# Optimization experiments

Measured on AMD Instinct MI355X. Metric: run time of the kernel, lower is better.

Reference implementation:

```python
import jax, jax.numpy as jnp
import numpy as np

NUM_UNITS = 64
IN_FEATURES = 256
OUT_FEATURES = 256


def _uw(x, w):
    # per-unit linear: x [B,U,I], w [U,I,O] -> [B,U,O]
    return jnp.einsum('bui,uio->buo', x, w)


def setup_inputs() -> dict:
    key = jax.random.key(0)
    ks = jax.random.split(key, 8)
    bound = float(np.sqrt(1.0 / OUT_FEATURES))
    U, I, O = NUM_UNITS, IN_FEATURES, OUT_FEATURES
    B = 256
    uni = lambda k, s: jax.random.uniform(k, s, jnp.float32, -bound, bound)
    return {
        'x': jax.random.normal(ks[0], (B, U, I), jnp.float32),
        'w_ir': uni(ks[1], (U, I, O)),
        'w_iz': uni(ks[2], (U, I, O)),
        'w_in': uni(ks[3], (U, I, O)),
        'w_hr': uni(ks[4], (U, O, O)),
        'w_hz': uni(ks[5], (U, O, O)),
        'w_hn': uni(ks[6], (U, O, O)),
        'hidden_init': uni(ks[7], (1, U, O)),
    }


def reference(x, w_ir, w_iz, w_in, w_hr, w_hz, w_hn, hidden_init):
    # hidden initialized by broadcasting hidden_init over batch (first call)
    h = jnp.broadcast_to(hidden_init, (x.shape[0],) + hidden_init.shape[1:])
    r = jax.nn.sigmoid(_uw(x, w_ir) + _uw(h, w_hr))
    z = jax.nn.sigmoid(_uw(x, w_iz) + _uw(h, w_hz))
    n = jnp.tanh(_uw(x, w_in) + r * _uw(h, w_hn))
    return (1.0 - z) * n + z * h
```

## Files before the change

### kernel.cpp

```cpp
#include <hip/hip_runtime.h>
#include <hip/hip_bf16.h>

#define UNITS 64
#define IFEAT 256
#define OFEAT 256

typedef __attribute__((ext_vector_type(8))) short v8s;
typedef __attribute__((ext_vector_type(4))) float v4f;

static __device__ __forceinline__ unsigned int pk2(float a, float b) {
    union { __hip_bfloat162 h; unsigned int u; } c;
    c.h = __float22bfloat162_rn(float2{a, b});
    return c.u;
}
static __device__ __forceinline__ v8s pk8(const float* r) {
    union { uint4 u4; v8s s8; } cv;
    cv.u4.x = pk2(r[0], r[1]);
    cv.u4.y = pk2(r[2], r[3]);
    cv.u4.z = pk2(r[4], r[5]);
    cv.u4.w = pk2(r[6], r[7]);
    return cv.s8;
}

static __device__ __forceinline__ float sigmoid_f(float x) {
    return 1.0f / (1.0f + __expf(-x));
}
static __device__ __forceinline__ float tanh_f(float x) {
    float ax = fabsf(x);
    float e = __expf(-2.0f * ax);
    float t = (1.0f - e) / (1.0f + e);
    return copysignf(t, x);
}

__global__ __launch_bounds__(512, 1) void gru_fused(
    const float* __restrict__ x,
    const float* __restrict__ wir,
    const float* __restrict__ wiz,
    const float* __restrict__ win,
    const float* __restrict__ whr,
    const float* __restrict__ whz,
    const float* __restrict__ whn,
    const float* __restrict__ hinit,
    float* __restrict__ out) {
    __shared__ unsigned short As[32][256][8];
    __shared__ unsigned short Ht[32][8];

    const int bid = blockIdx.x;
    const int loc = bid >> 3;
    const int u   = (bid & 7) * 8 + (loc >> 2);
    const int o0  = (loc & 3) * 64;

    const int t    = threadIdx.x;
    const int lane = t & 63;
    const int wv   = t >> 6;
    const int wm   = wv >> 2;
    const int wn   = wv & 3;
    const int lg   = lane >> 4;
    const int lr   = lane & 15;

    const float* WX[3] = {wir, wiz, win};
    const float* WH[3] = {whr, whz, whn};

    {
        const int kqA = lane >> 1;
        const int j0  = (lane & 1) * 4;
#pragma unroll
        for (int i = 0; i < 32; ++i) {
            const int row = wv * 32 + i;
            v4f q = *(const v4f*)(x + (size_t)row * (UNITS * IFEAT)
                                    + u * IFEAT + lane * 4);
            uint2 w;
            w.x = pk2(q[0], q[1]);
            w.y = pk2(q[2], q[3]);
            *(uint2*)&As[kqA][(row + kqA) & 255][j0] = w;
        }
    }
    if (t < 32) {
        const float* hp = hinit + u * IFEAT + t * 8;
        v4f q0 = *(const v4f*)hp;
        v4f q1 = *(const v4f*)(hp + 4);
        uint4 w;
        w.x = pk2(q0[0], q0[1]);
        w.y = pk2(q0[2], q0[3]);
        w.z = pk2(q1[0], q1[1]);
        w.w = pk2(q1[2], q1[3]);
        *(uint4*)&Ht[t][0] = w;
    }

    const size_t bcolofs = (size_t)u * (IFEAT * OFEAT) + o0 + wn * 16 + lr;

    float rbA[3][8], rbB[3][8];

#define LOADB(dst, s)                                                        \
    {                                                                        \
        const float* const* W = ((s) < 8) ? WX : WH;                         \
        const size_t boff = bcolofs + (size_t)(((s) & 7) * 4 + lg) * 8 * OFEAT; \
        _Pragma("unroll")                                                    \
        for (int g = 0; g < 3; ++g) {                                        \
            const float* p = W[g] + boff;                                    \
            _Pragma("unroll")                                                \
            for (int j = 0; j < 8; ++j) dst[g][j] = p[j * OFEAT];            \
        }                                                                    \
    }

    v4f acc[3][8];
    v4f acch[3];
#pragma unroll
    for (int g = 0; g < 3; ++g) {
#pragma unroll
        for (int mi = 0; mi < 8; ++mi)
            acc[g][mi] = (v4f){0.f, 0.f, 0.f, 0.f};
        acch[g] = (v4f){0.f, 0.f, 0.f, 0.f};
    }

    LOADB(rbA, 0);
    __syncthreads();

#pragma unroll
    for (int s = 0; s < 16; ++s) {
        if (s < 15) {
            if (s & 1) { LOADB(rbA, s + 1); }
            else       { LOADB(rbB, s + 1); }
        }
        const float (*rb)[8] = (s & 1) ? rbB : rbA;

        v8s bf[3];
#pragma unroll
        for (int g = 0; g < 3; ++g) bf[g] = pk8(rb[g]);

        const int kq = (s & 7) * 4 + lg;
        if (s < 8) {
#pragma unroll
            for (int mi = 0; mi < 8; ++mi) {
                v8s a = *(const v8s*)&As[kq][((wm * 128 + mi * 16 + lr) + kq) & 255][0];
#pragma unroll
                for (int g = 0; g < 3; ++g)
                    acc[g][mi] = __builtin_amdgcn_mfma_f32_16x16x32_bf16(
                        a, bf[g], acc[g][mi], 0, 0, 0);
            }
        } else {
            v8s a0h = *(const v8s*)&Ht[kq][0];
#pragma unroll
            for (int g = 0; g < 3; ++g)
                acch[g] = __builtin_amdgcn_mfma_f32_16x16x32_bf16(
                    a0h, bf[g], acch[g], 0, 0, 0);
        }
    }
#undef LOADB

    const int o = o0 + wn * 16 + lr;
    const float h0v = hinit[u * OFEAT + o];
    const float hr = acch[0][0];
    const float hz = acch[1][0];
    const float hn = acch[2][0];
#pragma unroll
    for (int mi = 0; mi < 8; ++mi) {
#pragma unroll
        for (int jj = 0; jj < 4; ++jj) {
            const int row = wm * 128 + mi * 16 + lg * 4 + jj;
            const float r = sigmoid_f(acc[0][mi][jj] + hr);
            const float z = sigmoid_f(acc[1][mi][jj] + hz);
            const float n = tanh_f(acc[2][mi][jj] + r * hn);
            out[(size_t)row * (UNITS * OFEAT) + u * OFEAT + o] =
                (1.0f - z) * n + z * h0v;
        }
    }
}

extern "C" void kernel_launch(void* const* d_in, const int* in_sizes, int n_in,
                              void* d_out, int out_size, void* d_ws, size_t ws_size,
                              hipStream_t stream) {
    const float* x     = (const float*)d_in[0];
    const float* w_ir  = (const float*)d_in[1];
    const float* w_iz  = (const float*)d_in[2];
    const float* w_in  = (const float*)d_in[3];
    const float* w_hr  = (const float*)d_in[4];
    const float* w_hz  = (const float*)d_in[5];
    const float* w_hn  = (const float*)d_in[6];
    const float* hinit = (const float*)d_in[7];
    float* out = (float*)d_out;

    gru_fused<<<dim3(256), dim3(512), 0, stream>>>(
        x, w_ir, w_iz, w_in, w_hr, w_hz, w_hn, hinit, out);
}
```

Before: 36.39 us.

## Retile blocks to 128 batch x 128 outputs and deepen weight prefetch pipeline

Each block now covers a 128-row batch half and a 128-column output half instead of all 256 rows and 64 columns. Every wave owns a distinct 16-column slice, so no two waves load the same weight columns and the shared A tile halves in size. Weight loads are prefetched two stages ahead, and the bf16 conversion moves after the MFMAs so it overlaps with them. In exchange, each x row is now loaded and converted by two blocks and register pressure is higher.

New measurement: 31.82 us. -12.6%, faster.

```diff
diff --git a/kernel.cpp b/kernel.cpp
--- a/kernel.cpp
+++ b/kernel.cpp
@@ -42,37 +42,61 @@
     const float* __restrict__ whn,
     const float* __restrict__ hinit,
     float* __restrict__ out) {
-    __shared__ unsigned short As[32][256][8];
+    __shared__ unsigned short As[32][128][8];
     __shared__ unsigned short Ht[32][8];
 
     const int bid = blockIdx.x;
-    const int loc = bid >> 3;
-    const int u   = (bid & 7) * 8 + (loc >> 2);
-    const int o0  = (loc & 3) * 64;
+    const int idx = bid >> 3;
+    const int u   = (bid & 7) * 8 + (idx >> 2);
+    const int rem = idx & 3;
+    const int b0  = (rem >> 1) * 128;
+    const int o0  = (rem & 1) * 128;
 
     const int t    = threadIdx.x;
     const int lane = t & 63;
     const int wv   = t >> 6;
-    const int wm   = wv >> 2;
-    const int wn   = wv & 3;
     const int lg   = lane >> 4;
     const int lr   = lane & 15;
 
     const float* WX[3] = {wir, wiz, win};
     const float* WH[3] = {whr, whz, whn};
 
+    const size_t bcolofs = (size_t)u * (IFEAT * OFEAT) + o0 + wv * 16 + lr;
+
+    float rbFa[3][8], rbFb[3][8];
+    v8s bfQa[3], bfQb[3];
+
+#define LOADB(dst, s)                                                        \
+    {                                                                        \
+        const float* const* W = ((s) < 8) ? WX : WH;                         \
+        const size_t boff = bcolofs + (size_t)(((s) & 7) * 4 + lg) * 8 * OFEAT; \
+        _Pragma("unroll")                                                    \
+        for (int g = 0; g < 3; ++g) {                                        \
+            const float* p = W[g] + boff;                                    \
+            _Pragma("unroll")                                                \
+            for (int j = 0; j < 8; ++j) dst[g][j] = p[j * OFEAT];            \
+        }                                                                    \
+    }
+#define CVTQ(dq, sr)                                                         \
+    {                                                                        \
+        _Pragma("unroll")                                                    \
+        for (int g = 0; g < 3; ++g) dq[g] = pk8(sr[g]);                      \
+    }
+
+    LOADB(rbFa, 0);
+    LOADB(rbFb, 1);
     {
         const int kqA = lane >> 1;
         const int j0  = (lane & 1) * 4;
 #pragma unroll
-        for (int i = 0; i < 32; ++i) {
-            const int row = wv * 32 + i;
-            v4f q = *(const v4f*)(x + (size_t)row * (UNITS * IFEAT)
+        for (int i = 0; i < 16; ++i) {
+            const int row = wv * 16 + i;
+            v4f q = *(const v4f*)(x + (size_t)(b0 + row) * (UNITS * IFEAT)
                                     + u * IFEAT + lane * 4);
             uint2 w;
             w.x = pk2(q[0], q[1]);
             w.y = pk2(q[2], q[3]);
-            *(uint2*)&As[kqA][(row + kqA) & 255][j0] = w;
+            *(uint2*)&As[kqA][(row + kqA) & 127][j0] = w;
         }
     }
     if (t < 32) {
@@ -87,68 +111,59 @@
         *(uint4*)&Ht[t][0] = w;
     }
 
-    const size_t bcolofs = (size_t)u * (IFEAT * OFEAT) + o0 + wn * 16 + lr;
-
-    float rbA[3][8], rbB[3][8];
-
-#define LOADB(dst, s)                                                        \
-    {                                                                        \
-        const float* const* W = ((s) < 8) ? WX : WH;                         \
-        const size_t boff = bcolofs + (size_t)(((s) & 7) * 4 + lg) * 8 * OFEAT; \
-        _Pragma("unroll")                                                    \
-        for (int g = 0; g < 3; ++g) {                                        \
-            const float* p = W[g] + boff;                                    \
-            _Pragma("unroll")                                                \
-            for (int j = 0; j < 8; ++j) dst[g][j] = p[j * OFEAT];            \
-        }                                                                    \
-    }
-
     v4f acc[3][8];
     v4f acch[3];
 #pragma unroll
-    for (int g = 0; g < 3; ++g) {
+    for (int g = 0; g < 3; ++g)
 #pragma unroll
         for (int mi = 0; mi < 8; ++mi)
             acc[g][mi] = (v4f){0.f, 0.f, 0.f, 0.f};
-        acch[g] = (v4f){0.f, 0.f, 0.f, 0.f};
-    }
-
-    LOADB(rbA, 0);
+
     __syncthreads();
+    CVTQ(bfQa, rbFa);
 
 #pragma unroll
     for (int s = 0; s < 16; ++s) {
-        if (s < 15) {
-            if (s & 1) { LOADB(rbA, s + 1); }
-            else       { LOADB(rbB, s + 1); }
-        }
-        const float (*rb)[8] = (s & 1) ? rbB : rbA;
-
-        v8s bf[3];
-#pragma unroll
-        for (int g = 0; g < 3; ++g) bf[g] = pk8(rb[g]);
+        if (s < 14) {
+            if (s & 1) { LOADB(rbFb, s + 2); }
+            else       { LOADB(rbFa, s + 2); }
+        }
 
         const int kq = (s & 7) * 4 + lg;
         if (s < 8) {
 #pragma unroll
             for (int mi = 0; mi < 8; ++mi) {
-                v8s a = *(const v8s*)&As[kq][((wm * 128 + mi * 16 + lr) + kq) & 255][0];
-#pragma unroll
-                for (int g = 0; g < 3; ++g)
+                v8s a = *(const v8s*)&As[kq][((mi * 16 + lr) + kq) & 127][0];
+#pragma unroll
+                for (int g = 0; g < 3; ++g) {
+                    const v8s bv = (s & 1) ? bfQb[g] : bfQa[g];
                     acc[g][mi] = __builtin_amdgcn_mfma_f32_16x16x32_bf16(
-                        a, bf[g], acc[g][mi], 0, 0, 0);
+                        a, bv, acc[g][mi], 0, 0, 0);
+                }
             }
         } else {
+            if (s == 8) {
+#pragma unroll
+                for (int g = 0; g < 3; ++g) acch[g] = (v4f){0.f, 0.f, 0.f, 0.f};
+            }
             v8s a0h = *(const v8s*)&Ht[kq][0];
 #pragma unroll
-            for (int g = 0; g < 3; ++g)
+            for (int g = 0; g < 3; ++g) {
+                const v8s bv = (s & 1) ? bfQb[g] : bfQa[g];
                 acch[g] = __builtin_amdgcn_mfma_f32_16x16x32_bf16(
-                    a0h, bf[g], acch[g], 0, 0, 0);
+                    a0h, bv, acch[g], 0, 0, 0);
+            }
+        }
+
+        if (s < 15) {
+            if (s & 1) { CVTQ(bfQa, rbFa); }
+            else       { CVTQ(bfQb, rbFb); }
         }
     }
 #undef LOADB
-
-    const int o = o0 + wn * 16 + lr;
+#undef CVTQ
+
+    const int o = o0 + wv * 16 + lr;
     const float h0v = hinit[u * OFEAT + o];
     const float hr = acch[0][0];
     const float hz = acch[1][0];
@@ -157,7 +172,7 @@
     for (int mi = 0; mi < 8; ++mi) {
 #pragma unroll
         for (int jj = 0; jj < 4; ++jj) {
-            const int row = wm * 128 + mi * 16 + lg * 4 + jj;
+            const int row = b0 + mi * 16 + lg * 4 + jj;
             const float r = sigmoid_f(acc[0][mi][jj] + hr);
             const float z = sigmoid_f(acc[1][mi][jj] + hz);
             const float n = tanh_f(acc[2][mi][jj] + r * hn);
```
